# Optimization experiments

Measured on AMD Instinct MI355X. Metric: run time of the kernel, lower is better.

Reference implementation:

```python
import jax, jax.numpy as jnp
import numpy as np

HK, HV, D, K = 32, 32, 128, 4   # key heads, value heads, head dim, conv kernel
B = 128                          # decoding batch (seq=1 per step)
QKV = (2 * HK + HV) * D          # 12288


def _l2norm(x, eps=1e-6):
    return x * jax.lax.rsqrt(jnp.sum(x * x, axis=-1, keepdims=True) + eps)


def setup_inputs() -> dict:
    key = jax.random.key(0)
    ks = jax.random.split(key, 8)
    return {
        "mixed_qkv": jax.random.normal(ks[0], (B, QKV), jnp.float32),
        "forget_gate": jax.random.normal(ks[1], (B, HV * D), jnp.float32),
        "beta": jax.random.normal(ks[2], (B, HV), jnp.float32),
        "conv_state": jax.random.normal(ks[3], (B, QKV, K - 1), jnp.float32),
        "conv_weights": jax.random.normal(ks[4], (QKV, K), jnp.float32) * 0.1,
        "ssm_state": jax.random.normal(ks[5], (B, HV, D, D), jnp.float32) * 0.1,
        "A_log": jax.random.normal(ks[6], (HV,), jnp.float32),
        "dt_bias": jax.random.normal(ks[7], (HV * D,), jnp.float32),
    }


def reference(mixed_qkv, forget_gate, beta, conv_state, conv_weights, ssm_state, A_log, dt_bias):
    # --- causal conv1d single-step update (causal_conv1d_update, silu, no bias) ---
    # window = [past K-1 inputs | current input] per channel
    window = jnp.concatenate([conv_state, mixed_qkv[:, :, None]], axis=2)  # [B, QKV, K]
    x = jax.nn.silu(jnp.einsum('bck,ck->bc', window, conv_weights))        # [B, QKV]

    # --- split q/k/v heads ---
    qkv = x.reshape(B, 2 * HK + HV, D)
    q, k, v = qkv[:, :HK], qkv[:, HK:2 * HK], qkv[:, 2 * HK:]

    # use_qk_l2norm_in_kernel=True; scale=None -> D**-0.5 folded into q
    q = _l2norm(q) * (D ** -0.5)
    k = _l2norm(k)

    # use_gate_in_kernel=True: fused KDA gate  g = -exp(A_log) * softplus(f + dt_bias)
    g = -jnp.exp(A_log)[None, :, None] * jax.nn.softplus(
        forget_gate.reshape(B, HV, D) + dt_bias.reshape(HV, D)[None]
    )  # [B, HV, D] log-decay per key dim
    b = jax.nn.sigmoid(beta)  # [B, HV] per-head write strength

    # --- gated delta-rule recurrent update (single decode step) ---
    S = ssm_state * jnp.exp(g)[..., None]                  # decay state along key dim
    kv_mem = jnp.einsum('bhk,bhkv->bhv', k, S)             # current memory readout
    delta = (v - kv_mem) * b[..., None]                    # delta-rule correction
    S = S + k[..., None] * delta[:, :, None, :]            # rank-1 state write
    o = jnp.einsum('bhk,bhkv->bhv', q, S)                  # [B, HV, D]
    return o
```

## Files before the change

kernel.cpp:

```cpp
#include <hip/hip_runtime.h>
#include <math.h>

#define NHK   32
#define NHV   32
#define DDIM  128
#define NB    128
#define QKVC  12288

typedef float f32x4 __attribute__((ext_vector_type(4)));

__device__ __forceinline__ float sigmoid_f(float x) { return 1.0f / (1.0f + expf(-x)); }
__device__ __forceinline__ float silu_f(float x)    { return x * sigmoid_f(x); }
__device__ __forceinline__ float softplus_f(float x){ return (x > 20.0f) ? x : log1pf(expf(x)); }

__global__ __launch_bounds__(256, 4)
void kda_decode_kernel(const float* __restrict__ mixed,
                       const float* __restrict__ fgate,
                       const float* __restrict__ beta,
                       const float* __restrict__ cstate,
                       const float* __restrict__ cweight,
                       const float* __restrict__ ssm,
                       const float* __restrict__ A_log,
                       const float* __restrict__ dt_bias,
                       float* __restrict__ out)
{
    const int bh  = blockIdx.x;
    const int b   = bh >> 5;
    const int h   = bh & 31;
    const int tid = threadIdx.x;

    __shared__ float w_q[DDIM], w_k[DDIM], v_s[DDIM];
    __shared__ float pq[8][DDIM], pk[8][DDIM];
    __shared__ float part[4][3];

    float cs_q[3], cs_k[3], cs_v[3];
    float4 cw_q = {0,0,0,0}, cw_k = {0,0,0,0}, cw_v = {0,0,0,0};
    float mx_q = 0.f, mx_k = 0.f, mx_v = 0.f, fg = 0.f, dtb = 0.f;
    cs_q[0]=cs_q[1]=cs_q[2]=0.f; cs_k[0]=cs_k[1]=cs_k[2]=0.f; cs_v[0]=cs_v[1]=cs_v[2]=0.f;

    const float betav = beta[b * NHV + h];
    const float alog  = A_log[h];

    if (tid < DDIM) {
        const int cq = h * DDIM + tid;
        const int ck = (NHK + h) * DDIM + tid;
        const int cv = (2 * NHK + h) * DDIM + tid;
        const size_t b3 = (size_t)b * QKVC * 3;
        const size_t b1 = (size_t)b * QKVC;

        #pragma unroll
        for (int j = 0; j < 3; ++j) {
            cs_q[j] = cstate[b3 + (size_t)cq * 3 + j];
            cs_k[j] = cstate[b3 + (size_t)ck * 3 + j];
            cs_v[j] = cstate[b3 + (size_t)cv * 3 + j];
        }
        cw_q = *reinterpret_cast<const float4*>(cweight + (size_t)cq * 4);
        cw_k = *reinterpret_cast<const float4*>(cweight + (size_t)ck * 4);
        cw_v = *reinterpret_cast<const float4*>(cweight + (size_t)cv * 4);
        mx_q = mixed[b1 + cq];
        mx_k = mixed[b1 + ck];
        mx_v = mixed[b1 + cv];
        fg   = fgate[(size_t)b * (NHV * DDIM) + h * DDIM + tid];
        dtb  = dt_bias[h * DDIM + tid];
    }

    float xq = 0.f, xk = 0.f, xv = 0.f;
    if (tid < DDIM) {
        xq = silu_f(cs_q[0]*cw_q.x + cs_q[1]*cw_q.y + cs_q[2]*cw_q.z + mx_q*cw_q.w);
        xk = silu_f(cs_k[0]*cw_k.x + cs_k[1]*cw_k.y + cs_k[2]*cw_k.z + mx_k*cw_k.w);
        xv = silu_f(cs_v[0]*cw_v.x + cs_v[1]*cw_v.y + cs_v[2]*cw_v.z + mx_v*cw_v.w);
    }

    float a0 = xq * xq, a1 = xk * xk, a2 = xq * xk;
    #pragma unroll
    for (int off = 32; off; off >>= 1) {
        a0 += __shfl_xor(a0, off);
        a1 += __shfl_xor(a1, off);
        a2 += __shfl_xor(a2, off);
    }
    const int wid = tid >> 6;
    if ((tid & 63) == 0) { part[wid][0] = a0; part[wid][1] = a1; part[wid][2] = a2; }
    __syncthreads();
    const float q2  = part[0][0] + part[1][0];
    const float k2  = part[0][1] + part[1][1];
    const float qkd = part[0][2] + part[1][2];

    const float dscale = 0.08838834764831845f;
    const float rq = rsqrtf(q2 + 1e-6f);
    const float rk = rsqrtf(k2 + 1e-6f);
    const float qk = qkd * rq * rk * dscale;
    const float bsig = sigmoid_f(betav);

    if (tid < DDIM) {
        const float g  = -expf(alog) * softplus_f(fg + dtb);
        const float eg = expf(g);
        w_q[tid] = xq * rq * dscale * eg;
        w_k[tid] = xk * rk * eg;
        v_s[tid] = xv;
    }
    __syncthreads();

    const float* Sb = ssm + (size_t)bh * (DDIM * DDIM);
    const int rp   = tid >> 5;
    const int col4 = (tid & 31) * 4;

    float4 accq = {0.f, 0.f, 0.f, 0.f};
    float4 acck = {0.f, 0.f, 0.f, 0.f};
    #pragma unroll 4
    for (int i = 0; i < 16; ++i) {
        const int row = i * 8 + rp;
        const f32x4 sv = __builtin_nontemporal_load(
            reinterpret_cast<const f32x4*>(Sb + (size_t)row * DDIM + col4));
        const float wq = w_q[row];
        const float wk = w_k[row];
        accq.x = fmaf(wq, sv.x, accq.x); accq.y = fmaf(wq, sv.y, accq.y);
        accq.z = fmaf(wq, sv.z, accq.z); accq.w = fmaf(wq, sv.w, accq.w);
        acck.x = fmaf(wk, sv.x, acck.x); acck.y = fmaf(wk, sv.y, acck.y);
        acck.z = fmaf(wk, sv.z, acck.z); acck.w = fmaf(wk, sv.w, acck.w);
    }
    *reinterpret_cast<float4*>(&pq[rp][col4]) = accq;
    *reinterpret_cast<float4*>(&pk[rp][col4]) = acck;
    __syncthreads();

    if (tid < DDIM) {
        float aq = 0.f, ak = 0.f;
        #pragma unroll
        for (int g = 0; g < 8; ++g) { aq += pq[g][tid]; ak += pk[g][tid]; }
        const float o = aq + qk * (v_s[tid] - ak) * bsig;
        out[(size_t)bh * DDIM + tid] = o;
    }
}

extern "C" void kernel_launch(void* const* d_in, const int* in_sizes, int n_in,
                              void* d_out, int out_size, void* d_ws, size_t ws_size,
                              hipStream_t stream) {
    const float* mixed   = (const float*)d_in[0];
    const float* fgate   = (const float*)d_in[1];
    const float* beta    = (const float*)d_in[2];
    const float* cstate  = (const float*)d_in[3];
    const float* cweight = (const float*)d_in[4];
    const float* ssm     = (const float*)d_in[5];
    const float* A_log   = (const float*)d_in[6];
    const float* dt_bias = (const float*)d_in[7];
    float* out = (float*)d_out;

    kda_decode_kernel<<<NB * NHV, 256, 0, stream>>>(
        mixed, fgate, beta, cstate, cweight, ssm, A_log, dt_bias, out);
}
```

Before: 364.7 us.

## Split into prep and streaming kernels with merged single-vector state contraction

Splits the fused kernel into a small prep kernel and a state-streaming kernel. The prep kernel does the conv, norms and gate and writes one combined weight vector (wq - c*wk) plus a bias (c*v) to workspace. The streaming kernel then needs only one matvec over the state instead of two. Each wave handles a whole head tile with a half-wave shuffle reduction, which removes the LDS partial-sum reductions and block syncs. In exchange it adds a second launch and a workspace round-trip, and the tile-to-wave mapping reads rows interleaved across the two half-waves.

```diff
diff --git a/kernel.cpp b/kernel.cpp
--- a/kernel.cpp
+++ b/kernel.cpp
@@ -6,6 +6,7 @@
 #define DDIM  128
 #define NB    128
 #define QKVC  12288
+#define NTILE (NB * NHV)
 
 typedef float f32x4 __attribute__((ext_vector_type(4)));
 
@@ -13,63 +14,50 @@
 __device__ __forceinline__ float silu_f(float x)    { return x * sigmoid_f(x); }
 __device__ __forceinline__ float softplus_f(float x){ return (x > 20.0f) ? x : log1pf(expf(x)); }
 
-__global__ __launch_bounds__(256, 4)
-void kda_decode_kernel(const float* __restrict__ mixed,
-                       const float* __restrict__ fgate,
-                       const float* __restrict__ beta,
-                       const float* __restrict__ cstate,
-                       const float* __restrict__ cweight,
-                       const float* __restrict__ ssm,
-                       const float* __restrict__ A_log,
-                       const float* __restrict__ dt_bias,
-                       float* __restrict__ out)
+__global__ __launch_bounds__(128)
+void kda_prep(const float* __restrict__ mixed,
+              const float* __restrict__ fgate,
+              const float* __restrict__ beta,
+              const float* __restrict__ cstate,
+              const float* __restrict__ cweight,
+              const float* __restrict__ A_log,
+              const float* __restrict__ dt_bias,
+              float* __restrict__ wb)
 {
     const int bh  = blockIdx.x;
     const int b   = bh >> 5;
     const int h   = bh & 31;
     const int tid = threadIdx.x;
 
-    __shared__ float w_q[DDIM], w_k[DDIM], v_s[DDIM];
-    __shared__ float pq[8][DDIM], pk[8][DDIM];
-    __shared__ float part[4][3];
+    __shared__ float part[2][3];
+
+    const int cq = h * DDIM + tid;
+    const int ck = (NHK + h) * DDIM + tid;
+    const int cv = (2 * NHK + h) * DDIM + tid;
+    const size_t b3 = (size_t)b * QKVC * 3;
+    const size_t b1 = (size_t)b * QKVC;
 
     float cs_q[3], cs_k[3], cs_v[3];
-    float4 cw_q = {0,0,0,0}, cw_k = {0,0,0,0}, cw_v = {0,0,0,0};
-    float mx_q = 0.f, mx_k = 0.f, mx_v = 0.f, fg = 0.f, dtb = 0.f;
-    cs_q[0]=cs_q[1]=cs_q[2]=0.f; cs_k[0]=cs_k[1]=cs_k[2]=0.f; cs_v[0]=cs_v[1]=cs_v[2]=0.f;
-
+    #pragma unroll
+    for (int j = 0; j < 3; ++j) {
+        cs_q[j] = cstate[b3 + (size_t)cq * 3 + j];
+        cs_k[j] = cstate[b3 + (size_t)ck * 3 + j];
+        cs_v[j] = cstate[b3 + (size_t)cv * 3 + j];
+    }
+    const float4 cw_q = *reinterpret_cast<const float4*>(cweight + (size_t)cq * 4);
+    const float4 cw_k = *reinterpret_cast<const float4*>(cweight + (size_t)ck * 4);
+    const float4 cw_v = *reinterpret_cast<const float4*>(cweight + (size_t)cv * 4);
+    const float mx_q = mixed[b1 + cq];
+    const float mx_k = mixed[b1 + ck];
+    const float mx_v = mixed[b1 + cv];
+    const float fg   = fgate[(size_t)b * (NHV * DDIM) + h * DDIM + tid];
+    const float dtb  = dt_bias[h * DDIM + tid];
     const float betav = beta[b * NHV + h];
     const float alog  = A_log[h];
 
-    if (tid < DDIM) {
-        const int cq = h * DDIM + tid;
-        const int ck = (NHK + h) * DDIM + tid;
-        const int cv = (2 * NHK + h) * DDIM + tid;
-        const size_t b3 = (size_t)b * QKVC * 3;
-        const size_t b1 = (size_t)b * QKVC;
-
-        #pragma unroll
-        for (int j = 0; j < 3; ++j) {
-            cs_q[j] = cstate[b3 + (size_t)cq * 3 + j];
-            cs_k[j] = cstate[b3 + (size_t)ck * 3 + j];
-            cs_v[j] = cstate[b3 + (size_t)cv * 3 + j];
-        }
-        cw_q = *reinterpret_cast<const float4*>(cweight + (size_t)cq * 4);
-        cw_k = *reinterpret_cast<const float4*>(cweight + (size_t)ck * 4);
-        cw_v = *reinterpret_cast<const float4*>(cweight + (size_t)cv * 4);
-        mx_q = mixed[b1 + cq];
-        mx_k = mixed[b1 + ck];
-        mx_v = mixed[b1 + cv];
-        fg   = fgate[(size_t)b * (NHV * DDIM) + h * DDIM + tid];
-        dtb  = dt_bias[h * DDIM + tid];
-    }
-
-    float xq = 0.f, xk = 0.f, xv = 0.f;
-    if (tid < DDIM) {
-        xq = silu_f(cs_q[0]*cw_q.x + cs_q[1]*cw_q.y + cs_q[2]*cw_q.z + mx_q*cw_q.w);
-        xk = silu_f(cs_k[0]*cw_k.x + cs_k[1]*cw_k.y + cs_k[2]*cw_k.z + mx_k*cw_k.w);
-        xv = silu_f(cs_v[0]*cw_v.x + cs_v[1]*cw_v.y + cs_v[2]*cw_v.z + mx_v*cw_v.w);
-    }
+    const float xq = silu_f(cs_q[0]*cw_q.x + cs_q[1]*cw_q.y + cs_q[2]*cw_q.z + mx_q*cw_q.w);
+    const float xk = silu_f(cs_k[0]*cw_k.x + cs_k[1]*cw_k.y + cs_k[2]*cw_k.z + mx_k*cw_k.w);
+    const float xv = silu_f(cs_v[0]*cw_v.x + cs_v[1]*cw_v.y + cs_v[2]*cw_v.z + mx_v*cw_v.w);
 
     float a0 = xq * xq, a1 = xk * xk, a2 = xq * xk;
     #pragma unroll
@@ -88,46 +76,78 @@
     const float dscale = 0.08838834764831845f;
     const float rq = rsqrtf(q2 + 1e-6f);
     const float rk = rsqrtf(k2 + 1e-6f);
-    const float qk = qkd * rq * rk * dscale;
-    const float bsig = sigmoid_f(betav);
+    const float c  = qkd * rq * rk * dscale * sigmoid_f(betav);
 
-    if (tid < DDIM) {
-        const float g  = -expf(alog) * softplus_f(fg + dtb);
-        const float eg = expf(g);
-        w_q[tid] = xq * rq * dscale * eg;
-        w_k[tid] = xk * rk * eg;
-        v_s[tid] = xv;
+    const float g  = -expf(alog) * softplus_f(fg + dtb);
+    const float eg = expf(g);
+    const float wq = xq * rq * dscale * eg;
+    const float wk = xk * rk * eg;
+
+    float* W = wb + (size_t)bh * 256;
+    W[tid]        = wq - c * wk;
+    W[DDIM + tid] = c * xv;
+}
+
+__global__ __launch_bounds__(256)
+void kda_stream(const float* __restrict__ ssm,
+                const float* __restrict__ wb,
+                float* __restrict__ out)
+{
+    const int wid  = threadIdx.x >> 6;
+    const int lane = threadIdx.x & 63;
+    const int tile = (blockIdx.x << 2) | wid;
+
+    const float* W  = wb  + (size_t)tile * 256;
+    const float* Sb = ssm + (size_t)tile * (DDIM * DDIM);
+    const float* base = Sb + lane * 4;
+
+    const int half = lane >> 5;
+    const int c4   = (lane & 31) * 4;
+
+    f32x4 acc0 = {0.f,0.f,0.f,0.f}, acc1 = {0.f,0.f,0.f,0.f};
+    f32x4 acc2 = {0.f,0.f,0.f,0.f}, acc3 = {0.f,0.f,0.f,0.f};
+
+    #pragma unroll 2
+    for (int i = 0; i < 64; i += 4) {
+        const f32x4 s0 = __builtin_nontemporal_load(reinterpret_cast<const f32x4*>(base + (size_t)(i+0) * 256));
+        const f32x4 s1 = __builtin_nontemporal_load(reinterpret_cast<const f32x4*>(base + (size_t)(i+1) * 256));
+        const f32x4 s2 = __builtin_nontemporal_load(reinterpret_cast<const f32x4*>(base + (size_t)(i+2) * 256));
+        const f32x4 s3 = __builtin_nontemporal_load(reinterpret_cast<const f32x4*>(base + (size_t)(i+3) * 256));
+        const float2 wp0 = *reinterpret_cast<const float2*>(W + 2*(i+0));
+        const float2 wp1 = *reinterpret_cast<const float2*>(W + 2*(i+1));
+        const float2 wp2 = *reinterpret_cast<const float2*>(W + 2*(i+2));
+        const float2 wp3 = *reinterpret_cast<const float2*>(W + 2*(i+3));
+        const float w0 = half ? wp0.y : wp0.x;
+        const float w1 = half ? wp1.y : wp1.x;
+        const float w2 = half ? wp2.y : wp2.x;
+        const float w3 = half ? wp3.y : wp3.x;
+        acc0.x = fmaf(w0, s0.x, acc0.x); acc0.y = fmaf(w0, s0.y, acc0.y);
+        acc0.z = fmaf(w0, s0.z, acc0.z); acc0.w = fmaf(w0, s0.w, acc0.w);
+        acc1.x = fmaf(w1, s1.x, acc1.x); acc1.y = fmaf(w1, s1.y, acc1.y);
+        acc1.z = fmaf(w1, s1.z, acc1.z); acc1.w = fmaf(w1, s1.w, acc1.w);
+        acc2.x = fmaf(w2, s2.x, acc2.x); acc2.y = fmaf(w2, s2.y, acc2.y);
+        acc2.z = fmaf(w2, s2.z, acc2.z); acc2.w = fmaf(w2, s2.w, acc2.w);
+        acc3.x = fmaf(w3, s3.x, acc3.x); acc3.y = fmaf(w3, s3.y, acc3.y);
+        acc3.z = fmaf(w3, s3.z, acc3.z); acc3.w = fmaf(w3, s3.w, acc3.w);
     }
-    __syncthreads();
 
-    const float* Sb = ssm + (size_t)bh * (DDIM * DDIM);
-    const int rp   = tid >> 5;
-    const int col4 = (tid & 31) * 4;
+    f32x4 acc;
+    acc.x = (acc0.x + acc1.x) + (acc2.x + acc3.x);
+    acc.y = (acc0.y + acc1.y) + (acc2.y + acc3.y);
+    acc.z = (acc0.z + acc1.z) + (acc2.z + acc3.z);
+    acc.w = (acc0.w + acc1.w) + (acc2.w + acc3.w);
 
-    float4 accq = {0.f, 0.f, 0.f, 0.f};
-    float4 acck = {0.f, 0.f, 0.f, 0.f};
-    #pragma unroll 4
-    for (int i = 0; i < 16; ++i) {
-        const int row = i * 8 + rp;
-        const f32x4 sv = __builtin_nontemporal_load(
-            reinterpret_cast<const f32x4*>(Sb + (size_t)row * DDIM + col4));
-        const float wq = w_q[row];
-        const float wk = w_k[row];
-        accq.x = fmaf(wq, sv.x, accq.x); accq.y = fmaf(wq, sv.y, accq.y);
-        accq.z = fmaf(wq, sv.z, accq.z); accq.w = fmaf(wq, sv.w, accq.w);
-        acck.x = fmaf(wk, sv.x, acck.x); acck.y = fmaf(wk, sv.y, acck.y);
-        acck.z = fmaf(wk, sv.z, acck.z); acck.w = fmaf(wk, sv.w, acck.w);
-    }
-    *reinterpret_cast<float4*>(&pq[rp][col4]) = accq;
-    *reinterpret_cast<float4*>(&pk[rp][col4]) = acck;
-    __syncthreads();
+    acc.x += __shfl_xor(acc.x, 32);
+    acc.y += __shfl_xor(acc.y, 32);
+    acc.z += __shfl_xor(acc.z, 32);
+    acc.w += __shfl_xor(acc.w, 32);
 
-    if (tid < DDIM) {
-        float aq = 0.f, ak = 0.f;
-        #pragma unroll
-        for (int g = 0; g < 8; ++g) { aq += pq[g][tid]; ak += pk[g][tid]; }
-        const float o = aq + qk * (v_s[tid] - ak) * bsig;
-        out[(size_t)bh * DDIM + tid] = o;
+    if (half == 0) {
+        const f32x4 bias = *reinterpret_cast<const f32x4*>(W + DDIM + c4);
+        f32x4 o;
+        o.x = acc.x + bias.x; o.y = acc.y + bias.y;
+        o.z = acc.z + bias.z; o.w = acc.w + bias.w;
+        *reinterpret_cast<f32x4*>(out + (size_t)tile * DDIM + c4) = o;
     }
 }
 
@@ -143,7 +163,9 @@
     const float* A_log   = (const float*)d_in[6];
     const float* dt_bias = (const float*)d_in[7];
     float* out = (float*)d_out;
+    float* wb  = (float*)d_ws;
 
-    kda_decode_kernel<<<NB * NHV, 256, 0, stream>>>(
-        mixed, fgate, beta, cstate, cweight, ssm, A_log, dt_bias, out);
+    kda_prep<<<NTILE, 128, 0, stream>>>(mixed, fgate, beta, cstate, cweight,
+                                        A_log, dt_bias, wb);
+    kda_stream<<<NTILE / 4, 256, 0, stream>>>(ssm, wb, out);
 }
```

Result: no change. 367.5 us (+0.8%).
